# Performance work log

Measured on AMD Instinct MI355X. Metric: run time of the kernel, lower is better.

## Reference

```python
import jax, jax.numpy as jnp
import numpy as np

P = 8          # patch_num_in == patch_num_out
R = 16         # patch_resolution (pixels per patch side)
C = 2          # dim_channel
D = 512        # dim_token
NH = 8         # nhead
DFF = 2048     # dim_feedforward
L = 6          # num_layers
PAIRS = 5      # demo_num
BS = 8
HW = P * R     # 128
S = PAIRS * 2 * P * P  # 640 tokens
EPS = 1e-5


def _patchify(x):
    # x: (N, c, H, W) -> (N, P*P, c*R*R)
    N, c, H, W = x.shape
    x = x.reshape(N, c, P, R, P, R).transpose(0, 2, 4, 1, 3, 5)
    return x.reshape(N, P * P, c * R * R)


def _depatchify(x, c):
    # x: (N, P*P, c*R*R) -> (N, c, P*R, P*R)
    N = x.shape[0]
    x = x.reshape(N, P, P, c, R, R).transpose(0, 3, 1, 4, 2, 5)
    return x.reshape(N, c, P * R, P * R)


def _ln(x, s, b):
    mu = jnp.mean(x, axis=-1, keepdims=True)
    var = jnp.mean(jnp.square(x - mu), axis=-1, keepdims=True)
    return (x - mu) * jax.lax.rsqrt(var + EPS) * s + b


def _block_lowtri_additive_mask(seq_len):
    blk = jnp.arange(seq_len) // (P * P)  # alternating init/end blocks of size P*P
    allowed = blk[:, None] >= blk[None, :]
    return jnp.where(allowed, 0.0, -jnp.inf).astype(jnp.float32)


def setup_inputs() -> dict:
    key = jax.random.key(0)
    ks = jax.random.split(key, 20)
    s = 0.02
    f32 = jnp.float32
    inp = {
        "init": jax.random.normal(ks[0], (BS, PAIRS, C, HW, HW), f32),
        "end": jax.random.normal(ks[1], (BS, PAIRS, C, HW, HW), f32),
        "c_mask": jnp.ones((BS, C), dtype=bool),
        "pre_W": (jax.random.normal(ks[2], (D, C * R * R), f32) * s),
        "pre_b": jnp.zeros((D,), f32),
        "post_W": (jax.random.normal(ks[3], (C * R * R, D), f32) * s),
        "post_b": jnp.zeros((C * R * R,), f32),
        "patch_pos": jax.random.normal(ks[4], (P * P, D), f32),
        "func_pos": jax.random.normal(ks[5], (PAIRS * 2, D), f32),
        "Wqkv": (jax.random.normal(ks[6], (L, 3 * D, D), f32) * s),
        "bqkv": jnp.zeros((L, 3 * D), f32),
        "Wo": (jax.random.normal(ks[7], (L, D, D), f32) * s),
        "bo": jnp.zeros((L, D), f32),
        "ln1_s": jnp.ones((L, D), f32),
        "ln1_b": jnp.zeros((L, D), f32),
        "ln2_s": jnp.ones((L, D), f32),
        "ln2_b": jnp.zeros((L, D), f32),
        "W1": (jax.random.normal(ks[8], (L, DFF, D), f32) * s),
        "b1": jnp.zeros((L, DFF), f32),
        "W2": (jax.random.normal(ks[9], (L, D, DFF), f32) * s),
        "b2": jnp.zeros((L, D), f32),
    }
    return inp


def _forward(init, end, pre_W, pre_b, post_W, post_b, patch_pos, func_pos,
             Wqkv, bqkv, Wo, bo, ln1_s, ln1_b, ln2_s, ln2_b, W1, b1, W2, b2):
    bs, pairs = init.shape[0], init.shape[1]
    # interleave (init, end) per pair: (bs, pairs, 2, c, h, w)
    x = jnp.concatenate([init[:, :, None], end[:, :, None]], axis=2)
    f = x.reshape(-1, C, HW, HW)
    f = _patchify(f)                                    # (N, P*P, C*R*R)
    f = f @ pre_W.T + pre_b                             # (N, P*P, D)
    f = f + patch_pos                                   # patch pos encoding
    f = f.reshape(bs, pairs * 2, P * P, D)
    f = f + func_pos[: pairs * 2][None, :, None, :]     # func pos encoding
    seq = pairs * 2 * P * P
    f = f.reshape(bs, seq, D)

    amask = _block_lowtri_additive_mask(seq)            # (S, S) additive
    dh = D // NH
    scale = 1.0 / np.sqrt(dh).astype(np.float32)

    for l in range(L):
        qkv = f @ Wqkv[l].T + bqkv[l]                   # (bs, S, 3D)
        q, k, v = jnp.split(qkv, 3, axis=-1)
        q = q.reshape(bs, seq, NH, dh).transpose(0, 2, 1, 3)
        k = k.reshape(bs, seq, NH, dh).transpose(0, 2, 1, 3)
        v = v.reshape(bs, seq, NH, dh).transpose(0, 2, 1, 3)
        scores = jnp.einsum('bhqd,bhkd->bhqk', q, k) * scale + amask
        attn = jax.nn.softmax(scores, axis=-1)
        o = jnp.einsum('bhqk,bhkd->bhqd', attn, v)
        o = o.transpose(0, 2, 1, 3).reshape(bs, seq, D)
        o = o @ Wo[l].T + bo[l]
        f = _ln(f + o, ln1_s[l], ln1_b[l])              # post-norm (PyTorch default)
        ff = jax.nn.gelu(f @ W1[l].T + b1[l], approximate=False) @ W2[l].T + b2[l]
        f = _ln(f + ff, ln2_s[l], ln2_b[l])

    f = f.reshape(bs, pairs, 2, P * P, D)[:, :, 0]      # read prediction off init slots
    f = f @ post_W.T + post_b                           # (bs, pairs, P*P, C*R*R)
    f = f.reshape(bs * pairs, P * P, C * R * R)
    f = _depatchify(f, C)
    return f.reshape(bs, pairs, C, HW, HW)


def reference(init, end, c_mask, pre_W, pre_b, post_W, post_b, patch_pos, func_pos,
              Wqkv, bqkv, Wo, bo, ln1_s, ln1_b, ln2_s, ln2_b, W1, b1, W2, b2):
    # c_mask is unpacked but unused by the original forward
    return _forward(init, end, pre_W, pre_b, post_W, post_b, patch_pos, func_pos,
                    Wqkv, bqkv, Wo, bo, ln1_s, ln1_b, ln2_s, ln2_b, W1, b1, W2, b2)
```

## Files before the change

### kernel.cpp

```cpp
#include <hip/hip_runtime.h>
#include <hip/hip_bf16.h>

#define BSZ 8
#define PAIRS 5
#define NCH 2
#define HWP 128
#define PP 64
#define DIM 512
#define NHEAD 8
#define DHEAD 64
#define DFF 2048
#define NLAYER 6
#define SEQ 640
#define NTOK (BSZ * SEQ)
#define FIN 10
#define MPOST (BSZ * PAIRS * PP)

typedef unsigned short u16;
typedef __bf16 bf16_t;
typedef __attribute__((ext_vector_type(8))) __bf16 bf16x8;
typedef __attribute__((ext_vector_type(8))) unsigned short u16x8;
typedef __attribute__((ext_vector_type(4))) float f32x4;
#define MFMA16(a, b, c) __builtin_amdgcn_mfma_f32_16x16x32_bf16(a, b, c, 0, 0, 0)

__device__ __forceinline__ u16 f2b(float x) {
  unsigned u = __float_as_uint(x);
  return (u16)((u + 0x7fffu + ((u >> 16) & 1u)) >> 16);
}

__device__ __forceinline__ float gelu_t(float x) {
  float y = 0.7978845608f * (x + 0.044715f * x * x * x);
  y = fminf(fmaxf(y, -10.f), 10.f);
  float e = __expf(2.f * y);
  return 0.5f * x * (1.f + (e - 1.f) / (e + 1.f));
}

__device__ __forceinline__ void dma16(const u16* g, void* l) {
  __builtin_amdgcn_global_load_lds(
      (const __attribute__((address_space(1))) void*)g,
      (__attribute__((address_space(3))) void*)l, 16, 0, 0);
}

#define W_QKV (3 * DIM * DIM)
#define W_O (DIM * DIM)
#define W_1 (DFF * DIM)
#define OFF_O W_QKV
#define OFF_1 (W_QKV + W_O)
#define OFF_2 (W_QKV + W_O + W_1)
#define W_ALL (W_QKV + W_O + 2 * W_1)
#define PREPOST (2 * DIM * DIM)
#define N_CVT (PREPOST + NLAYER * W_ALL)

__global__ __launch_bounds__(256) void k_cvt_all(const float* __restrict__ preW,
                                                 const float* __restrict__ postW,
                                                 const float* __restrict__ wq,
                                                 const float* __restrict__ wo,
                                                 const float* __restrict__ w1,
                                                 const float* __restrict__ w2,
                                                 u16* __restrict__ dst) {
  size_t i = ((size_t)blockIdx.x * 256 + threadIdx.x) * 8;
  const float* src;
  size_t off;
  if (i < DIM * DIM) { src = preW; off = i; }
  else if (i < PREPOST) { src = postW; off = i - DIM * DIM; }
  else {
    size_t j = i - PREPOST;
    int l = (int)(j / W_ALL);
    size_t r = j - (size_t)l * W_ALL;
    if (r < OFF_O) { src = wq + (size_t)l * W_QKV; off = r; }
    else if (r < OFF_1) { src = wo + (size_t)l * W_O; off = r - OFF_O; }
    else if (r < OFF_2) { src = w1 + (size_t)l * W_1; off = r - OFF_1; }
    else { src = w2 + (size_t)l * W_1; off = r - OFF_2; }
  }
  float4 v0 = *(const float4*)(src + off);
  float4 v1 = *(const float4*)(src + off + 4);
  u16x8 o;
  o[0] = f2b(v0.x); o[1] = f2b(v0.y); o[2] = f2b(v0.z); o[3] = f2b(v0.w);
  o[4] = f2b(v1.x); o[5] = f2b(v1.y); o[6] = f2b(v1.z); o[7] = f2b(v1.w);
  *(u16x8*)(dst + i) = o;
}

__global__ __launch_bounds__(256) void k_patchify(const float* __restrict__ init,
                                                  const float* __restrict__ endp,
                                                  u16* __restrict__ A) {
  int i = blockIdx.x * 256 + threadIdx.x;
  int d = i & 511;
  int g = i >> 9;
  int p = g & 63;
  int fi = (g >> 6) % FIN;
  int b = g / SEQ;
  int e = fi & 1;
  int pr = fi >> 1;
  int c = d >> 8;
  int r1 = (d >> 4) & 15;
  int r2 = d & 15;
  int row = ((p >> 3) << 4) + r1;
  int col = ((p & 7) << 4) + r2;
  const float* src = e ? endp : init;
  size_t off = ((size_t)((b * PAIRS + pr) * NCH + c) << 14) + (size_t)row * HWP + col;
  A[i] = f2b(src[off]);
}

template <int NT, int MODE>
__global__ __launch_bounds__(256) void k_mma(const u16* __restrict__ A,
                                             const u16* __restrict__ B,
                                             const float* __restrict__ bias,
                                             u16* __restrict__ outB,
                                             float* __restrict__ outP,
                                             float* __restrict__ outF,
                                             const float* __restrict__ pp,
                                             const float* __restrict__ fp,
                                             int M, int N, int K, int Kblk, int act) {
  constexpr int FJ = NT / 32;
  constexpr int NC = (4 + NT / 16) / 4;
  __shared__ __align__(16) bf16_t As[3][64][32];
  __shared__ __align__(16) bf16_t Bs[3][NT][32];
  const int t = threadIdx.x;
  const int w = t >> 6, lane = t & 63, quad = lane >> 4, l16 = lane & 15;
  int bx = blockIdx.x, by = blockIdx.y;
  if ((gridDim.y & 7) == 0) {
    int lin = bx + gridDim.x * by;
    int YT = gridDim.y >> 3;
    int xcd = lin & 7, slot = lin >> 3;
    by = xcd * YT + slot % YT;
    bx = slot / YT;
  }
  const int row0 = by << 6, col0 = bx * NT;
  const size_t kOff = (size_t)blockIdx.z * Kblk;
  const int mB = (w & 1) << 5;
  const int nB = (w >> 1) * (NT / 2);

  const u16* aP[4];
#pragma unroll
  for (int c = 0; c < 4; ++c) {
    int r = row0 + c * 16 + (lane >> 2);
    int g = r;
    if (MODE == 3) {
      int p = r & 63, pr = (r >> 6) % PAIRS, b = r / (PAIRS * PP);
      g = b * SEQ + pr * 128 + p;
    }
    aP[c] = A + (size_t)g * K + kOff + ((lane & 3) << 3);
  }
  const u16* bP = B + (size_t)(col0 + (lane >> 2)) * K + kOff + ((lane & 3) << 3);

  f32x4 acc[2][FJ];
#pragma unroll
  for (int i = 0; i < 2; ++i)
#pragma unroll
    for (int j = 0; j < FJ; ++j) acc[i][j] = (f32x4){0.f, 0.f, 0.f, 0.f};

  auto stage = [&](int bu, int kk) {
#pragma unroll
    for (int s = 0; s < NC; ++s) {
      int c = NC * w + s;
      if (c < 4) dma16(aP[c] + kk, &As[bu][c * 16][0]);
      else dma16(bP + (size_t)((c - 4) * 16) * K + kk, &Bs[bu][(c - 4) * 16][0]);
    }
  };

  const int iters = Kblk >> 5;
  stage(0, 0);
  stage(1, 32);
  for (int it = 0; it < iters; ++it) {
    const int cur = it % 3;
    if (it > 0) asm volatile("s_barrier" ::: "memory");
    if (it + 2 < iters) stage((it + 2) % 3, (it + 2) << 5);
    if (it + 2 < iters) {
      if (NC == 3) asm volatile("s_waitcnt vmcnt(6)" ::: "memory");
      else asm volatile("s_waitcnt vmcnt(4)" ::: "memory");
    } else if (it + 1 < iters) {
      if (NC == 3) asm volatile("s_waitcnt vmcnt(3)" ::: "memory");
      else asm volatile("s_waitcnt vmcnt(2)" ::: "memory");
    } else {
      asm volatile("s_waitcnt vmcnt(0)" ::: "memory");
    }
    asm volatile("s_barrier" ::: "memory");
    bf16x8 af[2], bfr[FJ];
#pragma unroll
    for (int i = 0; i < 2; ++i)
      af[i] = *(const bf16x8*)&As[cur][mB + i * 16 + l16][quad * 8];
#pragma unroll
    for (int j = 0; j < FJ; ++j)
      bfr[j] = *(const bf16x8*)&Bs[cur][nB + j * 16 + l16][quad * 8];
#pragma unroll
    for (int i = 0; i < 2; ++i)
#pragma unroll
      for (int j = 0; j < FJ; ++j) acc[i][j] = MFMA16(af[i], bfr[j], acc[i][j]);
  }

#pragma unroll
  for (int i = 0; i < 2; ++i)
#pragma unroll
    for (int reg = 0; reg < 4; ++reg) {
      int m = row0 + mB + i * 16 + quad * 4 + reg;
#pragma unroll
      for (int j = 0; j < FJ; ++j) {
        int n = col0 + nB + j * 16 + l16;
        float v = acc[i][j][reg];
        if (MODE == 0) {
          v += bias[n];
          if (act) v = gelu_t(v);
          outB[(size_t)m * N + n] = f2b(v);
        } else if (MODE == 1) {
          outP[(size_t)blockIdx.z * M * N + (size_t)m * N + n] = v;
        } else if (MODE == 2) {
          int p = m & 63, fi = (m >> 6) % FIN;
          v += bias[n] + pp[p * DIM + n] + fp[fi * DIM + n];
          outF[(size_t)m * N + n] = v;
          outB[(size_t)m * N + n] = f2b(v);
        } else {
          v += bias[n];
          int p = m & 63, pr = (m >> 6) % PAIRS, b = m / (PAIRS * PP);
          int c = n >> 8, r1 = (n >> 4) & 15, r2 = n & 15;
          int row = ((p >> 3) << 4) + r1, col = ((p & 7) << 4) + r2;
          size_t off = ((size_t)((b * PAIRS + pr) * NCH + c) << 14) +
                       (size_t)row * HWP + col;
          outF[off] = v;
        }
      }
    }
}

__global__ __launch_bounds__(256) void k_attn(const u16* __restrict__ qkv,
                                              u16* __restrict__ o) {
  __shared__ bf16_t Qs[64][72];
  __shared__ bf16_t Ks[64][72];
  __shared__ bf16_t Vs[64][72];
  __shared__ bf16_t Ps[64][72];
  const int t = threadIdx.x;
  const int w = t >> 6, lane = t & 63, quad = lane >> 4, l16 = lane & 15;
  const int qblk = blockIdx.x, h = blockIdx.y, b = blockIdx.z;
  const int q0 = qblk << 6;
  const u16* base = qkv + (size_t)b * SEQ * (3 * DIM);
  const int sr = t >> 2;
  const int sd = (t & 3) << 4;
  const int rowB = 3 * DIM;
  {
    const u16* qp = base + (size_t)(q0 + sr) * rowB + h * DHEAD + sd;
    *(bf16x8*)&Qs[sr][sd] = *(const bf16x8*)(const void*)qp;
    *(bf16x8*)&Qs[sr][sd + 8] = *(const bf16x8*)(const void*)(qp + 8);
  }
  __syncthreads();
  bf16x8 aQ0 = *(const bf16x8*)&Qs[w * 16 + l16][quad * 8];
  bf16x8 aQ1 = *(const bf16x8*)&Qs[w * 16 + l16][32 + quad * 8];
  f32x4 accO[4];
#pragma unroll
  for (int j = 0; j < 4; ++j) accO[j] = (f32x4){0.f, 0.f, 0.f, 0.f};
  float mSt[4] = {-1e30f, -1e30f, -1e30f, -1e30f};
  float lSt[4] = {0.f, 0.f, 0.f, 0.f};
  const int ntile = qblk + 1;
  const u16* kp0 = base + (size_t)sr * rowB + DIM + h * DHEAD + sd;
  const u16* vp0 = base + (size_t)sr * rowB + 2 * DIM + h * DHEAD + sd;
  bf16x8 kR0 = *(const bf16x8*)(const void*)kp0;
  bf16x8 kR1 = *(const bf16x8*)(const void*)(kp0 + 8);
  bf16x8 vR0 = *(const bf16x8*)(const void*)vp0;
  bf16x8 vR1 = *(const bf16x8*)(const void*)(vp0 + 8);
  for (int kt = 0; kt < ntile; ++kt) {
    *(bf16x8*)&Ks[sr][sd] = kR0;
    *(bf16x8*)&Ks[sr][sd + 8] = kR1;
#pragma unroll
    for (int e = 0; e < 8; ++e) Vs[sd + e][sr] = vR0[e];
#pragma unroll
    for (int e = 0; e < 8; ++e) Vs[sd + 8 + e][sr] = vR1[e];
    if (kt + 1 < ntile) {
      const u16* kp = kp0 + (size_t)(kt + 1) * 64 * rowB;
      const u16* vp = vp0 + (size_t)(kt + 1) * 64 * rowB;
      kR0 = *(const bf16x8*)(const void*)kp;
      kR1 = *(const bf16x8*)(const void*)(kp + 8);
      vR0 = *(const bf16x8*)(const void*)vp;
      vR1 = *(const bf16x8*)(const void*)(vp + 8);
    }
    __syncthreads();
    f32x4 s[4];
#pragma unroll
    for (int j = 0; j < 4; ++j) {
      bf16x8 b0 = *(const bf16x8*)&Ks[j * 16 + l16][quad * 8];
      bf16x8 b1 = *(const bf16x8*)&Ks[j * 16 + l16][32 + quad * 8];
      s[j] = (f32x4){0.f, 0.f, 0.f, 0.f};
      s[j] = MFMA16(aQ0, b0, s[j]);
      s[j] = MFMA16(aQ1, b1, s[j]);
      s[j] *= 0.125f;
    }
#pragma unroll
    for (int reg = 0; reg < 4; ++reg) {
      float mx = fmaxf(fmaxf(s[0][reg], s[1][reg]), fmaxf(s[2][reg], s[3][reg]));
      mx = fmaxf(mx, __shfl_xor(mx, 1));
      mx = fmaxf(mx, __shfl_xor(mx, 2));
      mx = fmaxf(mx, __shfl_xor(mx, 4));
      mx = fmaxf(mx, __shfl_xor(mx, 8));
      float mNew = fmaxf(mSt[reg], mx);
      float alpha = __expf(mSt[reg] - mNew);
      mSt[reg] = mNew;
      float rs = 0.f;
#pragma unroll
      for (int j = 0; j < 4; ++j) {
        float p = __expf(s[j][reg] - mNew);
        s[j][reg] = p;
        rs += p;
      }
      rs += __shfl_xor(rs, 1);
      rs += __shfl_xor(rs, 2);
      rs += __shfl_xor(rs, 4);
      rs += __shfl_xor(rs, 8);
      lSt[reg] = lSt[reg] * alpha + rs;
#pragma unroll
      for (int j = 0; j < 4; ++j) accO[j][reg] *= alpha;
    }
#pragma unroll
    for (int j = 0; j < 4; ++j)
#pragma unroll
      for (int reg = 0; reg < 4; ++reg)
        *(u16*)&Ps[w * 16 + quad * 4 + reg][j * 16 + l16] = f2b(s[j][reg]);
    __syncthreads();
    bf16x8 aP0 = *(const bf16x8*)&Ps[w * 16 + l16][quad * 8];
    bf16x8 aP1 = *(const bf16x8*)&Ps[w * 16 + l16][32 + quad * 8];
#pragma unroll
    for (int jd = 0; jd < 4; ++jd) {
      bf16x8 b0 = *(const bf16x8*)&Vs[jd * 16 + l16][quad * 8];
      bf16x8 b1 = *(const bf16x8*)&Vs[jd * 16 + l16][32 + quad * 8];
      accO[jd] = MFMA16(aP0, b0, accO[jd]);
      accO[jd] = MFMA16(aP1, b1, accO[jd]);
    }
    __syncthreads();
  }
#pragma unroll
  for (int reg = 0; reg < 4; ++reg) {
    float inv = 1.0f / lSt[reg];
    int row = q0 + w * 16 + quad * 4 + reg;
#pragma unroll
    for (int jd = 0; jd < 4; ++jd)
      o[((size_t)(b * SEQ + row)) * DIM + h * DHEAD + jd * 16 + l16] =
          f2b(accO[jd][reg] * inv);
  }
}

__global__ __launch_bounds__(256) void k_red_ln(const float* __restrict__ part, int KS,
                                                const float* __restrict__ bias,
                                                float* __restrict__ f,
                                                u16* __restrict__ fb,
                                                const float* __restrict__ s,
                                                const float* __restrict__ bvec) {
  const int row = blockIdx.x;
  const int t = threadIdx.x;
  const size_t base = (size_t)row * DIM;
  float x0 = f[base + t] + bias[t];
  float x1 = f[base + t + 256] + bias[t + 256];
  for (int z = 0; z < KS; ++z) {
    x0 += part[(size_t)z * NTOK * DIM + base + t];
    x1 += part[(size_t)z * NTOK * DIM + base + t + 256];
  }
  float sum = x0 + x1;
  float sq = x0 * x0 + x1 * x1;
#pragma unroll
  for (int off = 32; off; off >>= 1) {
    sum += __shfl_xor(sum, off);
    sq += __shfl_xor(sq, off);
  }
  __shared__ float rs[4], rq[4];
  const int w = t >> 6, lane = t & 63;
  if (lane == 0) { rs[w] = sum; rq[w] = sq; }
  __syncthreads();
  float tot = rs[0] + rs[1] + rs[2] + rs[3];
  float tq2 = rq[0] + rq[1] + rq[2] + rq[3];
  float mu = tot * (1.0f / 512.0f);
  float var = tq2 * (1.0f / 512.0f) - mu * mu;
  float rstd = rsqrtf(var + 1e-5f);
  float v0 = (x0 - mu) * rstd * s[t] + bvec[t];
  float v1 = (x1 - mu) * rstd * s[t + 256] + bvec[t + 256];
  f[base + t] = v0;
  f[base + t + 256] = v1;
  fb[base + t] = f2b(v0);
  fb[base + t + 256] = f2b(v1);
}

extern "C" void kernel_launch(void* const* d_in, const int* in_sizes, int n_in,
                              void* d_out, int out_size, void* d_ws, size_t ws_size,
                              hipStream_t stream) {
  const float* init = (const float*)d_in[0];
  const float* endp = (const float*)d_in[1];
  const float* pre_W = (const float*)d_in[3];
  const float* pre_b = (const float*)d_in[4];
  const float* post_W = (const float*)d_in[5];
  const float* post_b = (const float*)d_in[6];
  const float* patch_pos = (const float*)d_in[7];
  const float* func_pos = (const float*)d_in[8];
  const float* Wqkv = (const float*)d_in[9];
  const float* bqkv = (const float*)d_in[10];
  const float* Wo = (const float*)d_in[11];
  const float* bo = (const float*)d_in[12];
  const float* ln1_s = (const float*)d_in[13];
  const float* ln1_b = (const float*)d_in[14];
  const float* ln2_s = (const float*)d_in[15];
  const float* ln2_b = (const float*)d_in[16];
  const float* W1 = (const float*)d_in[17];
  const float* b1 = (const float*)d_in[18];
  const float* W2 = (const float*)d_in[19];
  const float* b2 = (const float*)d_in[20];
  float* out = (float*)d_out;

  char* p = (char*)d_ws;
  float* buf_f = (float*)p;    p += (size_t)NTOK * DIM * 4;
  u16* buf_fb = (u16*)p;       p += (size_t)NTOK * DIM * 2;
  u16* buf_attn = (u16*)p;     p += (size_t)NTOK * DIM * 2;
  u16* shared_b = (u16*)p;     p += (size_t)NTOK * DFF * 2;
  u16* wAll = (u16*)p;         p += (size_t)N_CVT * 2;
  float* partial = (float*)p;
  u16* buf_patch = shared_b;
  u16* buf_qkv = shared_b;
  u16* buf_hid = shared_b;
  u16* wPre = wAll;
  u16* wPost = wAll + DIM * DIM;
  u16* wL = wAll + PREPOST;

  dim3 blk(256);
  const int elems = NTOK * DIM;

  k_cvt_all<<<N_CVT / (256 * 8), blk, 0, stream>>>(pre_W, post_W, Wqkv, Wo, W1, W2,
                                                   wAll);
  k_patchify<<<elems / 256, blk, 0, stream>>>(init, endp, buf_patch);
  k_mma<64, 2><<<dim3(8, 80, 1), blk, 0, stream>>>(
      buf_patch, wPre, pre_b, buf_fb, nullptr, buf_f, patch_pos, func_pos,
      NTOK, DIM, DIM, DIM, 0);

  for (int l = 0; l < NLAYER; ++l) {
    u16* wB = wL + (size_t)l * W_ALL;
    k_mma<128, 0><<<dim3(12, 80, 1), blk, 0, stream>>>(
        buf_fb, wB, bqkv + (size_t)l * 3 * DIM, buf_qkv, nullptr, nullptr, nullptr,
        nullptr, NTOK, 3 * DIM, DIM, DIM, 0);
    k_attn<<<dim3(SEQ / 64, NHEAD, BSZ), blk, 0, stream>>>(buf_qkv, buf_attn);
    k_mma<64, 1><<<dim3(8, 80, 1), blk, 0, stream>>>(
        buf_attn, wB + OFF_O, nullptr, nullptr, partial, nullptr, nullptr, nullptr,
        NTOK, DIM, DIM, DIM, 0);
    k_red_ln<<<NTOK, blk, 0, stream>>>(partial, 1, bo + (size_t)l * DIM, buf_f,
                                       buf_fb, ln1_s + (size_t)l * DIM,
                                       ln1_b + (size_t)l * DIM);
    k_mma<128, 0><<<dim3(16, 80, 1), blk, 0, stream>>>(
        buf_fb, wB + OFF_1, b1 + (size_t)l * DFF, buf_hid, nullptr, nullptr, nullptr,
        nullptr, NTOK, DFF, DIM, DIM, 1);
    k_mma<64, 1><<<dim3(8, 80, 1), blk, 0, stream>>>(
        buf_hid, wB + OFF_2, nullptr, nullptr, partial, nullptr, nullptr, nullptr,
        NTOK, DIM, DFF, DFF, 0);
    k_red_ln<<<NTOK, blk, 0, stream>>>(partial, 1, b2 + (size_t)l * DIM, buf_f,
                                       buf_fb, ln2_s + (size_t)l * DIM,
                                       ln2_b + (size_t)l * DIM);
  }

  k_mma<64, 3><<<dim3(8, 40, 1), blk, 0, stream>>>(
      buf_fb, wPost, post_b, nullptr, nullptr, out, nullptr, nullptr,
      MPOST, DIM, DIM, DIM, 0);
}
```

Before: 943.2 us.

## Compute only init-slot query rows in final transformer layer

In the last layer, attention runs only over the query blocks for the init slots, and the out-projection, layernorms and FFN process only those gathered rows, because only they feed the output projection. Split-K plumbing is removed from the GEMM kernel. The residual layernorm kernel is vectorized to handle two rows per block with float4 accesses and optional row gathering. This adds extra workspace buffers and separate code paths for the final layer.

```diff
diff --git a/kernel.cpp b/kernel.cpp
--- a/kernel.cpp
+++ b/kernel.cpp
@@ -20,6 +20,7 @@
 typedef __bf16 bf16_t;
 typedef __attribute__((ext_vector_type(8))) __bf16 bf16x8;
 typedef __attribute__((ext_vector_type(8))) unsigned short u16x8;
+typedef __attribute__((ext_vector_type(4))) unsigned short u16x4;
 typedef __attribute__((ext_vector_type(4))) float f32x4;
 #define MFMA16(a, b, c) __builtin_amdgcn_mfma_f32_16x16x32_bf16(a, b, c, 0, 0, 0)
 
@@ -101,7 +102,7 @@
   A[i] = f2b(src[off]);
 }
 
-template <int NT, int MODE>
+template <int NT, int MODE, int GATHER>
 __global__ __launch_bounds__(256) void k_mma(const u16* __restrict__ A,
                                              const u16* __restrict__ B,
                                              const float* __restrict__ bias,
@@ -110,7 +111,7 @@
                                              float* __restrict__ outF,
                                              const float* __restrict__ pp,
                                              const float* __restrict__ fp,
-                                             int M, int N, int K, int Kblk, int act) {
+                                             int M, int N, int K, int act) {
   constexpr int FJ = NT / 32;
   constexpr int NC = (4 + NT / 16) / 4;
   __shared__ __align__(16) bf16_t As[3][64][32];
@@ -126,7 +127,6 @@
     bx = slot / YT;
   }
   const int row0 = by << 6, col0 = bx * NT;
-  const size_t kOff = (size_t)blockIdx.z * Kblk;
   const int mB = (w & 1) << 5;
   const int nB = (w >> 1) * (NT / 2);
 
@@ -135,13 +135,13 @@
   for (int c = 0; c < 4; ++c) {
     int r = row0 + c * 16 + (lane >> 2);
     int g = r;
-    if (MODE == 3) {
+    if (GATHER) {
       int p = r & 63, pr = (r >> 6) % PAIRS, b = r / (PAIRS * PP);
       g = b * SEQ + pr * 128 + p;
     }
-    aP[c] = A + (size_t)g * K + kOff + ((lane & 3) << 3);
-  }
-  const u16* bP = B + (size_t)(col0 + (lane >> 2)) * K + kOff + ((lane & 3) << 3);
+    aP[c] = A + (size_t)g * K + ((lane & 3) << 3);
+  }
+  const u16* bP = B + (size_t)(col0 + (lane >> 2)) * K + ((lane & 3) << 3);
 
   f32x4 acc[2][FJ];
 #pragma unroll
@@ -158,7 +158,7 @@
     }
   };
 
-  const int iters = Kblk >> 5;
+  const int iters = K >> 5;
   stage(0, 0);
   stage(1, 32);
   for (int it = 0; it < iters; ++it) {
@@ -202,7 +202,7 @@
           if (act) v = gelu_t(v);
           outB[(size_t)m * N + n] = f2b(v);
         } else if (MODE == 1) {
-          outP[(size_t)blockIdx.z * M * N + (size_t)m * N + n] = v;
+          outP[(size_t)m * N + n] = v;
         } else if (MODE == 2) {
           int p = m & 63, fi = (m >> 6) % FIN;
           v += bias[n] + pp[p * DIM + n] + fp[fi * DIM + n];
@@ -222,14 +222,14 @@
 }
 
 __global__ __launch_bounds__(256) void k_attn(const u16* __restrict__ qkv,
-                                              u16* __restrict__ o) {
+                                              u16* __restrict__ o, int qmul) {
   __shared__ bf16_t Qs[64][72];
   __shared__ bf16_t Ks[64][72];
   __shared__ bf16_t Vs[64][72];
   __shared__ bf16_t Ps[64][72];
   const int t = threadIdx.x;
   const int w = t >> 6, lane = t & 63, quad = lane >> 4, l16 = lane & 15;
-  const int qblk = blockIdx.x, h = blockIdx.y, b = blockIdx.z;
+  const int qblk = blockIdx.x * qmul, h = blockIdx.y, b = blockIdx.z;
   const int q0 = qblk << 6;
   const u16* base = qkv + (size_t)b * SEQ * (3 * DIM);
   const int sr = t >> 2;
@@ -334,23 +334,29 @@
   }
 }
 
-__global__ __launch_bounds__(256) void k_red_ln(const float* __restrict__ part, int KS,
+template <int GIN>
+__global__ __launch_bounds__(256) void k_red_ln(const float* __restrict__ part,
                                                 const float* __restrict__ bias,
-                                                float* __restrict__ f,
-                                                u16* __restrict__ fb,
+                                                const float* __restrict__ f_in,
+                                                float* __restrict__ f_out,
+                                                u16* __restrict__ fb_out,
                                                 const float* __restrict__ s,
                                                 const float* __restrict__ bvec) {
-  const int row = blockIdx.x;
   const int t = threadIdx.x;
-  const size_t base = (size_t)row * DIM;
-  float x0 = f[base + t] + bias[t];
-  float x1 = f[base + t + 256] + bias[t + 256];
-  for (int z = 0; z < KS; ++z) {
-    x0 += part[(size_t)z * NTOK * DIM + base + t];
-    x1 += part[(size_t)z * NTOK * DIM + base + t + 256];
-  }
-  float sum = x0 + x1;
-  float sq = x0 * x0 + x1 * x1;
+  const int half = t >> 7;
+  const int r = blockIdx.x * 2 + half;
+  const int c = (t & 127) * 4;
+  int g = r;
+  if (GIN) {
+    int p = r & 63, pr = (r >> 6) % PAIRS, b = r / (PAIRS * PP);
+    g = b * SEQ + pr * 128 + p;
+  }
+  float4 x = *(const float4*)(f_in + (size_t)g * DIM + c);
+  float4 pa = *(const float4*)(part + (size_t)r * DIM + c);
+  float4 bi = *(const float4*)(bias + c);
+  x.x += pa.x + bi.x; x.y += pa.y + bi.y; x.z += pa.z + bi.z; x.w += pa.w + bi.w;
+  float sum = x.x + x.y + x.z + x.w;
+  float sq = x.x * x.x + x.y * x.y + x.z * x.z + x.w * x.w;
 #pragma unroll
   for (int off = 32; off; off >>= 1) {
     sum += __shfl_xor(sum, off);
@@ -360,17 +366,22 @@
   const int w = t >> 6, lane = t & 63;
   if (lane == 0) { rs[w] = sum; rq[w] = sq; }
   __syncthreads();
-  float tot = rs[0] + rs[1] + rs[2] + rs[3];
-  float tq2 = rq[0] + rq[1] + rq[2] + rq[3];
+  float tot = rs[half * 2] + rs[half * 2 + 1];
+  float tq2 = rq[half * 2] + rq[half * 2 + 1];
   float mu = tot * (1.0f / 512.0f);
   float var = tq2 * (1.0f / 512.0f) - mu * mu;
   float rstd = rsqrtf(var + 1e-5f);
-  float v0 = (x0 - mu) * rstd * s[t] + bvec[t];
-  float v1 = (x1 - mu) * rstd * s[t + 256] + bvec[t + 256];
-  f[base + t] = v0;
-  f[base + t + 256] = v1;
-  fb[base + t] = f2b(v0);
-  fb[base + t + 256] = f2b(v1);
+  float4 sv = *(const float4*)(s + c);
+  float4 bv = *(const float4*)(bvec + c);
+  float4 o;
+  o.x = (x.x - mu) * rstd * sv.x + bv.x;
+  o.y = (x.y - mu) * rstd * sv.y + bv.y;
+  o.z = (x.z - mu) * rstd * sv.z + bv.z;
+  o.w = (x.w - mu) * rstd * sv.w + bv.w;
+  *(float4*)(f_out + (size_t)r * DIM + c) = o;
+  u16x4 ob;
+  ob[0] = f2b(o.x); ob[1] = f2b(o.y); ob[2] = f2b(o.z); ob[3] = f2b(o.w);
+  *(u16x4*)(fb_out + (size_t)r * DIM + c) = ob;
 }
 
 extern "C" void kernel_launch(void* const* d_in, const int* in_sizes, int n_in,
@@ -404,7 +415,9 @@
   u16* buf_attn = (u16*)p;     p += (size_t)NTOK * DIM * 2;
   u16* shared_b = (u16*)p;     p += (size_t)NTOK * DFF * 2;
   u16* wAll = (u16*)p;         p += (size_t)N_CVT * 2;
-  float* partial = (float*)p;
+  float* partial = (float*)p;  p += (size_t)NTOK * DIM * 4;
+  float* buf_fc = (float*)p;   p += (size_t)MPOST * DIM * 4;
+  u16* buf_fbc = (u16*)p;      p += (size_t)MPOST * DIM * 2;
   u16* buf_patch = shared_b;
   u16* buf_qkv = shared_b;
   u16* buf_hid = shared_b;
@@ -418,34 +431,57 @@
   k_cvt_all<<<N_CVT / (256 * 8), blk, 0, stream>>>(pre_W, post_W, Wqkv, Wo, W1, W2,
                                                    wAll);
   k_patchify<<<elems / 256, blk, 0, stream>>>(init, endp, buf_patch);
-  k_mma<64, 2><<<dim3(8, 80, 1), blk, 0, stream>>>(
+  k_mma<64, 2, 0><<<dim3(8, 80), blk, 0, stream>>>(
       buf_patch, wPre, pre_b, buf_fb, nullptr, buf_f, patch_pos, func_pos,
-      NTOK, DIM, DIM, DIM, 0);
+      NTOK, DIM, DIM, 0);
 
   for (int l = 0; l < NLAYER; ++l) {
     u16* wB = wL + (size_t)l * W_ALL;
-    k_mma<128, 0><<<dim3(12, 80, 1), blk, 0, stream>>>(
+    k_mma<128, 0, 0><<<dim3(12, 80), blk, 0, stream>>>(
         buf_fb, wB, bqkv + (size_t)l * 3 * DIM, buf_qkv, nullptr, nullptr, nullptr,
-        nullptr, NTOK, 3 * DIM, DIM, DIM, 0);
-    k_attn<<<dim3(SEQ / 64, NHEAD, BSZ), blk, 0, stream>>>(buf_qkv, buf_attn);
-    k_mma<64, 1><<<dim3(8, 80, 1), blk, 0, stream>>>(
-        buf_attn, wB + OFF_O, nullptr, nullptr, partial, nullptr, nullptr, nullptr,
-        NTOK, DIM, DIM, DIM, 0);
-    k_red_ln<<<NTOK, blk, 0, stream>>>(partial, 1, bo + (size_t)l * DIM, buf_f,
-                                       buf_fb, ln1_s + (size_t)l * DIM,
-                                       ln1_b + (size_t)l * DIM);
-    k_mma<128, 0><<<dim3(16, 80, 1), blk, 0, stream>>>(
-        buf_fb, wB + OFF_1, b1 + (size_t)l * DFF, buf_hid, nullptr, nullptr, nullptr,
-        nullptr, NTOK, DFF, DIM, DIM, 1);
-    k_mma<64, 1><<<dim3(8, 80, 1), blk, 0, stream>>>(
-        buf_hid, wB + OFF_2, nullptr, nullptr, partial, nullptr, nullptr, nullptr,
-        NTOK, DIM, DFF, DFF, 0);
-    k_red_ln<<<NTOK, blk, 0, stream>>>(partial, 1, b2 + (size_t)l * DIM, buf_f,
-                                       buf_fb, ln2_s + (size_t)l * DIM,
-                                       ln2_b + (size_t)l * DIM);
-  }
-
-  k_mma<64, 3><<<dim3(8, 40, 1), blk, 0, stream>>>(
-      buf_fb, wPost, post_b, nullptr, nullptr, out, nullptr, nullptr,
-      MPOST, DIM, DIM, DIM, 0);
-}
+        nullptr, NTOK, 3 * DIM, DIM, 0);
+    if (l < NLAYER - 1) {
+      k_attn<<<dim3(SEQ / 64, NHEAD, BSZ), blk, 0, stream>>>(buf_qkv, buf_attn, 1);
+      k_mma<64, 1, 0><<<dim3(8, 80), blk, 0, stream>>>(
+          buf_attn, wB + OFF_O, nullptr, nullptr, partial, nullptr, nullptr, nullptr,
+          NTOK, DIM, DIM, 0);
+      k_red_ln<0><<<NTOK / 2, blk, 0, stream>>>(partial, bo + (size_t)l * DIM,
+                                                buf_f, buf_f, buf_fb,
+                                                ln1_s + (size_t)l * DIM,
+                                                ln1_b + (size_t)l * DIM);
+      k_mma<128, 0, 0><<<dim3(16, 80), blk, 0, stream>>>(
+          buf_fb, wB + OFF_1, b1 + (size_t)l * DFF, buf_hid, nullptr, nullptr,
+          nullptr, nullptr, NTOK, DFF, DIM, 1);
+      k_mma<64, 1, 0><<<dim3(8, 80), blk, 0, stream>>>(
+          buf_hid, wB + OFF_2, nullptr, nullptr, partial, nullptr, nullptr, nullptr,
+          NTOK, DIM, DFF, 0);
+      k_red_ln<0><<<NTOK / 2, blk, 0, stream>>>(partial, b2 + (size_t)l * DIM,
+                                                buf_f, buf_f, buf_fb,
+                                                ln2_s + (size_t)l * DIM,
+                                                ln2_b + (size_t)l * DIM);
+    } else {
+      k_attn<<<dim3(SEQ / 128, NHEAD, BSZ), blk, 0, stream>>>(buf_qkv, buf_attn, 2);
+      k_mma<64, 1, 1><<<dim3(8, 40), blk, 0, stream>>>(
+          buf_attn, wB + OFF_O, nullptr, nullptr, partial, nullptr, nullptr, nullptr,
+          MPOST, DIM, DIM, 0);
+      k_red_ln<1><<<MPOST / 2, blk, 0, stream>>>(partial, bo + (size_t)l * DIM,
+                                                 buf_f, buf_fc, buf_fbc,
+                                                 ln1_s + (size_t)l * DIM,
+                                                 ln1_b + (size_t)l * DIM);
+      k_mma<128, 0, 0><<<dim3(16, 40), blk, 0, stream>>>(
+          buf_fbc, wB + OFF_1, b1 + (size_t)l * DFF, buf_hid, nullptr, nullptr,
+          nullptr, nullptr, MPOST, DFF, DIM, 1);
+      k_mma<64, 1, 0><<<dim3(8, 40), blk, 0, stream>>>(
+          buf_hid, wB + OFF_2, nullptr, nullptr, partial, nullptr, nullptr, nullptr,
+          MPOST, DIM, DFF, 0);
+      k_red_ln<0><<<MPOST / 2, blk, 0, stream>>>(partial, b2 + (size_t)l * DIM,
+                                                 buf_fc, buf_fc, buf_fbc,
+                                                 ln2_s + (size_t)l * DIM,
+                                                 ln2_b + (size_t)l * DIM);
+    }
+  }
+
+  k_mma<64, 3, 0><<<dim3(8, 40), blk, 0, stream>>>(
+      buf_fbc, wPost, post_b, nullptr, nullptr, out, nullptr, nullptr,
+      MPOST, DIM, DIM, 0);
+}
```

New measurement: 904.2 us. 4.1% less time.
